# Performance work log

Hardware: AMD Instinct MI355X
Metric: run time of the kernel (lower is better)

Reference implementation:

```python
import jax, jax.numpy as jnp
import numpy as np

GROUP = 32  # values per quantization group (per-group scale)

def setup_inputs() -> dict:
    key = jax.random.key(0)
    k1, k2, k3, k4 = jax.random.split(key, 4)
    B, S, IN, OUT = 4, 2048, 4096, 4096
    x = jax.random.normal(k1, (B, S, IN), dtype=jnp.float32)
    # packed 4-bit weights: each int32 byte-value in [0,256) holds two nibbles
    w_packed = jax.random.randint(k2, (OUT, IN // 2), 0, 256, dtype=jnp.int32)
    scales = jax.random.uniform(k3, (OUT, IN // GROUP), dtype=jnp.float32) * 0.02 + 0.001
    bias = jax.random.normal(k4, (OUT,), dtype=jnp.float32)
    return {"x": x, "w_packed": w_packed, "scales": scales, "bias": bias}

def _dequantize(w_packed, scales):
    # w_packed: [OUT, IN//2] int32 bytes, scales: [OUT, IN//GROUP]
    OUT = w_packed.shape[0]
    low = w_packed & 0xF
    high = (w_packed >> 4) & 0xF
    q = jnp.stack([low, high], axis=-1).reshape(OUT, -1)  # [OUT, IN]
    qf = q.astype(jnp.float32) - 8.0  # signed 4-bit centered at 8
    qg = qf.reshape(OUT, scales.shape[1], GROUP)
    w = qg * scales[:, :, None]
    return w.reshape(OUT, -1)  # [OUT, IN]

def reference(x, w_packed, scales, bias):
    # dequantize weights then F.linear: y = x @ W^T + b
    W = _dequantize(w_packed, scales)  # [OUT, IN]
    y = jnp.einsum('bsi,oi->bso', x, W) + bias
    return y
```

## Files before the change

### kernel.cpp

```cpp
#include <hip/hip_runtime.h>
#include <stdint.h>

#define M_TOT 8192
#define K_TOT 4096
#define N_TOT 4096
#define GROUPQ 32

#define BM 256
#define BN 256
#define BK 32
#define NT (K_TOT / BK)

typedef __bf16 bf16x8 __attribute__((ext_vector_type(8)));
typedef float f32x4 __attribute__((ext_vector_type(4)));
typedef unsigned short u16;
typedef unsigned short u16x8 __attribute__((ext_vector_type(8)));

__device__ __forceinline__ u16 f2bf_rne(float f) {
  union { float f; uint32_t u; } v; v.f = f;
  uint32_t u = v.u;
  uint32_t r = (u + 0x7FFFu + ((u >> 16) & 1u)) >> 16;
  return (u16)r;
}

__global__ void cvt_x_kernel(const float* __restrict__ x, u16* __restrict__ xb, int n8) {
  int stride = gridDim.x * blockDim.x;
  for (int i = blockIdx.x * blockDim.x + threadIdx.x; i < n8; i += stride) {
    const float4* p = (const float4*)(x + (size_t)i * 8);
    float4 a = p[0];
    float4 b = p[1];
    u16x8 o;
    o[0] = f2bf_rne(a.x); o[1] = f2bf_rne(a.y); o[2] = f2bf_rne(a.z); o[3] = f2bf_rne(a.w);
    o[4] = f2bf_rne(b.x); o[5] = f2bf_rne(b.y); o[6] = f2bf_rne(b.z); o[7] = f2bf_rne(b.w);
    *(u16x8*)(xb + (size_t)i * 8) = o;
  }
}

__global__ void dequant_w_kernel(const int* __restrict__ wp, const float* __restrict__ sc,
                                 u16* __restrict__ wb) {
  const int KH = K_TOT / 2;
  const int total = N_TOT * KH / 8;
  int stride = gridDim.x * blockDim.x;
  for (int t = blockIdx.x * blockDim.x + threadIdx.x; t < total; t += stride) {
    int base = t * 8;
    int o = base >> 11;
    int ci = base & 2047;
    int e0 = ci * 2;
    float scale = sc[o * (K_TOT / GROUPQ) + (e0 >> 5)];
    int4 p0 = *(const int4*)(wp + base);
    int4 p1 = *(const int4*)(wp + base + 4);
    int v[8] = {p0.x, p0.y, p0.z, p0.w, p1.x, p1.y, p1.z, p1.w};
    u16x8 oA, oB;
#pragma unroll
    for (int j = 0; j < 8; ++j) {
      float lo = (float)((v[j] & 0xF) - 8) * scale;
      float hi = (float)(((v[j] >> 4) & 0xF) - 8) * scale;
      u16 lob = f2bf_rne(lo), hib = f2bf_rne(hi);
      if (j < 4) { oA[2 * j] = lob; oA[2 * j + 1] = hib; }
      else       { oB[2 * (j - 4)] = lob; oB[2 * (j - 4) + 1] = hib; }
    }
    u16* dst = wb + (size_t)o * K_TOT + e0;
    *(u16x8*)dst = oA;
    *(u16x8*)(dst + 8) = oB;
  }
}

__global__ __launch_bounds__(512, 2) void gemm_bf16_kernel(
    const u16* __restrict__ A, const u16* __restrict__ Bt,
    const float* __restrict__ bias, float* __restrict__ C) {
  __shared__ alignas(16) u16 sA[3][BM * BK];
  __shared__ alignas(16) u16 sB[3][BN * BK];

  const int ntn = N_TOT / BN;
  int wg = blockIdx.x, nwg = gridDim.x;
  int cpx = nwg >> 3;
  int swz = (wg & 7) * cpx + (wg >> 3);
  int bm = swz / ntn, bn = swz % ntn;

  int tid = threadIdx.x, wid = tid >> 6, lane = tid & 63;
  int wr = wid >> 2, wc = wid & 3;

  int srow0 = (wid * 2) * 16 + (lane >> 2);
  int srow1 = (wid * 2 + 1) * 16 + (lane >> 2);
  int cl = lane & 3;
  int gch0 = (cl ^ ((srow0 >> 1) & 3)) * 8;
  int gch1 = (cl ^ ((srow1 >> 1) & 3)) * 8;
  const u16* aS0 = A + (size_t)(bm * BM + srow0) * K_TOT + gch0;
  const u16* aS1 = A + (size_t)(bm * BM + srow1) * K_TOT + gch1;
  const u16* bS0 = Bt + (size_t)(bn * BN + srow0) * K_TOT + gch0;
  const u16* bS1 = Bt + (size_t)(bn * BN + srow1) * K_TOT + gch1;
  int ldst0 = (wid * 2) * 16 * BK;
  int ldst1 = (wid * 2 + 1) * 16 * BK;

  auto stageA = [&](int ke, int b) {
    __builtin_amdgcn_global_load_lds(
        (const __attribute__((address_space(1))) uint32_t*)(aS0 + ke),
        (__attribute__((address_space(3))) uint32_t*)(&sA[b][ldst0]), 16, 0, 0);
    __builtin_amdgcn_global_load_lds(
        (const __attribute__((address_space(1))) uint32_t*)(aS1 + ke),
        (__attribute__((address_space(3))) uint32_t*)(&sA[b][ldst1]), 16, 0, 0);
  };
  auto stageB = [&](int ke, int b) {
    __builtin_amdgcn_global_load_lds(
        (const __attribute__((address_space(1))) uint32_t*)(bS0 + ke),
        (__attribute__((address_space(3))) uint32_t*)(&sB[b][ldst0]), 16, 0, 0);
    __builtin_amdgcn_global_load_lds(
        (const __attribute__((address_space(1))) uint32_t*)(bS1 + ke),
        (__attribute__((address_space(3))) uint32_t*)(&sB[b][ldst1]), 16, 0, 0);
  };

  int rr = lane & 15, rc = lane >> 4;
  int xorv = (rc ^ ((rr >> 1) & 3)) * 8;
  int abase = (wr * 128 + rr) * BK + xorv;
  int bbase = (wc * 64 + rr) * BK + xorv;

  f32x4 acc[8][4] = {};

  stageA(0, 0); stageB(0, 0);
  stageA(BK, 1); stageB(BK, 1);
  asm volatile("s_waitcnt vmcnt(4)" ::: "memory");
  __builtin_amdgcn_s_barrier();

  for (int t = 0; t < NT; ++t) {
    int bt = t % 3;
    int bs = (t + 2) % 3;
    int ks = (t + 2) * BK;
    const u16* cA = sA[bt];
    const u16* cB = sB[bt];
    bool pf = (t + 2) < NT;

    bf16x8 bfr[4], af[4];
#pragma unroll
    for (int n = 0; n < 4; ++n) bfr[n] = *(const bf16x8*)(cB + bbase + n * 16 * BK);
#pragma unroll
    for (int m = 0; m < 4; ++m) af[m] = *(const bf16x8*)(cA + abase + m * 16 * BK);
    if (pf) stageA(ks, bs);
    __builtin_amdgcn_s_barrier();
    asm volatile("s_waitcnt lgkmcnt(0)" ::: "memory");
    __builtin_amdgcn_sched_barrier(0);
    __builtin_amdgcn_s_setprio(1);
#pragma unroll
    for (int m = 0; m < 4; ++m)
#pragma unroll
      for (int n = 0; n < 4; ++n)
        acc[m][n] = __builtin_amdgcn_mfma_f32_16x16x32_bf16(af[m], bfr[n], acc[m][n], 0, 0, 0);
    __builtin_amdgcn_s_setprio(0);
    __builtin_amdgcn_s_barrier();

#pragma unroll
    for (int m = 0; m < 4; ++m) af[m] = *(const bf16x8*)(cA + abase + (m + 4) * 16 * BK);
    if (pf) stageB(ks, bs);
    __builtin_amdgcn_s_barrier();
    asm volatile("s_waitcnt lgkmcnt(0)" ::: "memory");
    __builtin_amdgcn_sched_barrier(0);
    __builtin_amdgcn_s_setprio(1);
#pragma unroll
    for (int m = 0; m < 4; ++m)
#pragma unroll
      for (int n = 0; n < 4; ++n)
        acc[m + 4][n] = __builtin_amdgcn_mfma_f32_16x16x32_bf16(af[m], bfr[n], acc[m + 4][n], 0, 0, 0);
    __builtin_amdgcn_s_setprio(0);
    if (pf) { asm volatile("s_waitcnt vmcnt(4)" ::: "memory"); }
    else    { asm volatile("s_waitcnt vmcnt(0)" ::: "memory"); }
    __builtin_amdgcn_s_barrier();
  }

  int col = lane & 15;
  int rb = (lane >> 4) * 4;
#pragma unroll
  for (int n = 0; n < 4; ++n) {
    int gn = bn * BN + wc * 64 + n * 16 + col;
    float bsv = bias[gn];
#pragma unroll
    for (int m = 0; m < 8; ++m) {
      int gm = bm * BM + wr * 128 + m * 16 + rb;
#pragma unroll
      for (int j = 0; j < 4; ++j)
        C[(size_t)(gm + j) * N_TOT + gn] = acc[m][n][j] + bsv;
    }
  }
}

__global__ void fill_kernel(float* p, int n, float v) {
  int stride = gridDim.x * blockDim.x;
  for (int i = blockIdx.x * blockDim.x + threadIdx.x; i < n; i += stride) p[i] = v;
}

extern "C" void kernel_launch(void* const* d_in, const int* in_sizes, int n_in,
                              void* d_out, int out_size, void* d_ws, size_t ws_size,
                              hipStream_t stream) {
  const float* x = (const float*)d_in[0];
  const int* wp = (const int*)d_in[1];
  const float* sc = (const float*)d_in[2];
  const float* bias = (const float*)d_in[3];
  float* out = (float*)d_out;

  size_t xb_bytes = (size_t)M_TOT * K_TOT * 2;
  size_t wb_bytes = (size_t)N_TOT * K_TOT * 2;
  if (ws_size < xb_bytes + wb_bytes) {
    fill_kernel<<<2048, 256, 0, stream>>>(out, out_size, 12345.0f);
    return;
  }
  u16* xb = (u16*)d_ws;
  u16* wb = (u16*)((char*)d_ws + xb_bytes);

  cvt_x_kernel<<<2048, 256, 0, stream>>>(x, xb, M_TOT * K_TOT / 8);
  dequant_w_kernel<<<2048, 256, 0, stream>>>(wp, sc, wb);
  gemm_bf16_kernel<<<(M_TOT / BM) * (N_TOT / BN), 512, 0, stream>>>(xb, wb, bias, out);
}
```

Before: 313.3 us.

## Deepen GEMM LDS pipeline to four stages with register double-buffered fragments

```diff
diff --git a/kernel.cpp b/kernel.cpp
--- a/kernel.cpp
+++ b/kernel.cpp
@@ -68,8 +68,8 @@
 __global__ __launch_bounds__(512, 2) void gemm_bf16_kernel(
     const u16* __restrict__ A, const u16* __restrict__ Bt,
     const float* __restrict__ bias, float* __restrict__ C) {
-  __shared__ alignas(16) u16 sA[3][BM * BK];
-  __shared__ alignas(16) u16 sB[3][BN * BK];
+  __shared__ alignas(16) u16 sA[4][BM * BK];
+  __shared__ alignas(16) u16 sB[4][BN * BK];
 
   const int ntn = N_TOT / BN;
   int wg = blockIdx.x, nwg = gridDim.x;
@@ -118,51 +118,54 @@
 
   stageA(0, 0); stageB(0, 0);
   stageA(BK, 1); stageB(BK, 1);
-  asm volatile("s_waitcnt vmcnt(4)" ::: "memory");
+  stageA(2 * BK, 2); stageB(2 * BK, 2);
+  asm volatile("s_waitcnt vmcnt(8)" ::: "memory");
   __builtin_amdgcn_s_barrier();
 
+  bf16x8 afA[4], bfrA[4], afB[4], afN[4], bfrN[4];
+#pragma unroll
+  for (int n = 0; n < 4; ++n) bfrA[n] = *(const bf16x8*)(sB[0] + bbase + n * 16 * BK);
+#pragma unroll
+  for (int m = 0; m < 4; ++m) afA[m] = *(const bf16x8*)(sA[0] + abase + m * 16 * BK);
+
   for (int t = 0; t < NT; ++t) {
-    int bt = t % 3;
-    int bs = (t + 2) % 3;
-    int ks = (t + 2) * BK;
-    const u16* cA = sA[bt];
-    const u16* cB = sB[bt];
-    bool pf = (t + 2) < NT;
-
-    bf16x8 bfr[4], af[4];
-#pragma unroll
-    for (int n = 0; n < 4; ++n) bfr[n] = *(const bf16x8*)(cB + bbase + n * 16 * BK);
-#pragma unroll
-    for (int m = 0; m < 4; ++m) af[m] = *(const bf16x8*)(cA + abase + m * 16 * BK);
-    if (pf) stageA(ks, bs);
+    const u16* cA = sA[t & 3];
+    const u16* cB = sB[t & 3];
+    const u16* nA = sA[(t + 1) & 3];
+    const u16* nB = sB[(t + 1) & 3];
+    int bs = (t + 3) & 3;
+    int ks = ((t + 3 < NT) ? (t + 3) : (NT - 1)) * BK;
+    (void)cB;
+
     __builtin_amdgcn_s_barrier();
-    asm volatile("s_waitcnt lgkmcnt(0)" ::: "memory");
-    __builtin_amdgcn_sched_barrier(0);
+    stageA(ks, bs);
+#pragma unroll
+    for (int m = 0; m < 4; ++m) afB[m] = *(const bf16x8*)(cA + abase + (m + 4) * 16 * BK);
     __builtin_amdgcn_s_setprio(1);
 #pragma unroll
     for (int m = 0; m < 4; ++m)
 #pragma unroll
       for (int n = 0; n < 4; ++n)
-        acc[m][n] = __builtin_amdgcn_mfma_f32_16x16x32_bf16(af[m], bfr[n], acc[m][n], 0, 0, 0);
+        acc[m][n] = __builtin_amdgcn_mfma_f32_16x16x32_bf16(afA[m], bfrA[n], acc[m][n], 0, 0, 0);
     __builtin_amdgcn_s_setprio(0);
+
+    asm volatile("s_waitcnt vmcnt(6)" ::: "memory");
     __builtin_amdgcn_s_barrier();
-
-#pragma unroll
-    for (int m = 0; m < 4; ++m) af[m] = *(const bf16x8*)(cA + abase + (m + 4) * 16 * BK);
-    if (pf) stageB(ks, bs);
-    __builtin_amdgcn_s_barrier();
-    asm volatile("s_waitcnt lgkmcnt(0)" ::: "memory");
-    __builtin_amdgcn_sched_barrier(0);
+    stageB(ks, bs);
+#pragma unroll
+    for (int n = 0; n < 4; ++n) bfrN[n] = *(const bf16x8*)(nB + bbase + n * 16 * BK);
+#pragma unroll
+    for (int m = 0; m < 4; ++m) afN[m] = *(const bf16x8*)(nA + abase + m * 16 * BK);
     __builtin_amdgcn_s_setprio(1);
 #pragma unroll
     for (int m = 0; m < 4; ++m)
 #pragma unroll
       for (int n = 0; n < 4; ++n)
-        acc[m + 4][n] = __builtin_amdgcn_mfma_f32_16x16x32_bf16(af[m], bfr[n], acc[m + 4][n], 0, 0, 0);
+        acc[m + 4][n] = __builtin_amdgcn_mfma_f32_16x16x32_bf16(afB[m], bfrA[n], acc[m + 4][n], 0, 0, 0);
     __builtin_amdgcn_s_setprio(0);
-    if (pf) { asm volatile("s_waitcnt vmcnt(4)" ::: "memory"); }
-    else    { asm volatile("s_waitcnt vmcnt(0)" ::: "memory"); }
-    __builtin_amdgcn_s_barrier();
+
+#pragma unroll
+    for (int i = 0; i < 4; ++i) { afA[i] = afN[i]; bfrA[i] = bfrN[i]; }
   }
 
   int col = lane & 15;
```

Measured after the change: 397.0 us. +26.7%, slower.

## Switch GEMM to 32x32x16 MFMA tiles and single-phase K-loop

Applied to the files above, without the earlier changes.

```diff
diff --git a/kernel.cpp b/kernel.cpp
--- a/kernel.cpp
+++ b/kernel.cpp
@@ -12,7 +12,7 @@
 #define NT (K_TOT / BK)
 
 typedef __bf16 bf16x8 __attribute__((ext_vector_type(8)));
-typedef float f32x4 __attribute__((ext_vector_type(4)));
+typedef float f32x16 __attribute__((ext_vector_type(16)));
 typedef unsigned short u16;
 typedef unsigned short u16x8 __attribute__((ext_vector_type(8)));
 
@@ -109,12 +109,15 @@
         (__attribute__((address_space(3))) uint32_t*)(&sB[b][ldst1]), 16, 0, 0);
   };
 
-  int rr = lane & 15, rc = lane >> 4;
-  int xorv = (rc ^ ((rr >> 1) & 3)) * 8;
-  int abase = (wr * 128 + rr) * BK + xorv;
-  int bbase = (wc * 64 + rr) * BK + xorv;
-
-  f32x4 acc[8][4] = {};
+  int rl = lane & 31;
+  int kx = lane >> 5;
+  int rx = (lane >> 1) & 3;
+  int abase = (wr * 128 + rl) * BK;
+  int bbase = (wc * 64 + rl) * BK;
+  int ch0 = ((0 * 2 + kx) ^ rx) * 8;
+  int ch1 = ((1 * 2 + kx) ^ rx) * 8;
+
+  f32x16 acc[4][2] = {};
 
   stageA(0, 0); stageB(0, 0);
   stageA(BK, 1); stageB(BK, 1);
@@ -129,54 +132,51 @@
     const u16* cB = sB[bt];
     bool pf = (t + 2) < NT;
 
-    bf16x8 bfr[4], af[4];
-#pragma unroll
-    for (int n = 0; n < 4; ++n) bfr[n] = *(const bf16x8*)(cB + bbase + n * 16 * BK);
-#pragma unroll
-    for (int m = 0; m < 4; ++m) af[m] = *(const bf16x8*)(cA + abase + m * 16 * BK);
-    if (pf) stageA(ks, bs);
-    __builtin_amdgcn_s_barrier();
+    if (pf) { stageA(ks, bs); stageB(ks, bs); }
+
+    bf16x8 af[4][2], bfr[2][2];
+#pragma unroll
+    for (int m = 0; m < 4; ++m) {
+      af[m][0] = *(const bf16x8*)(cA + abase + m * 32 * BK + ch0);
+      af[m][1] = *(const bf16x8*)(cA + abase + m * 32 * BK + ch1);
+    }
+#pragma unroll
+    for (int n = 0; n < 2; ++n) {
+      bfr[n][0] = *(const bf16x8*)(cB + bbase + n * 32 * BK + ch0);
+      bfr[n][1] = *(const bf16x8*)(cB + bbase + n * 32 * BK + ch1);
+    }
+
     asm volatile("s_waitcnt lgkmcnt(0)" ::: "memory");
     __builtin_amdgcn_sched_barrier(0);
     __builtin_amdgcn_s_setprio(1);
 #pragma unroll
-    for (int m = 0; m < 4; ++m)
-#pragma unroll
-      for (int n = 0; n < 4; ++n)
-        acc[m][n] = __builtin_amdgcn_mfma_f32_16x16x32_bf16(af[m], bfr[n], acc[m][n], 0, 0, 0);
+    for (int kk = 0; kk < 2; ++kk)
+#pragma unroll
+      for (int m = 0; m < 4; ++m)
+#pragma unroll
+        for (int n = 0; n < 2; ++n)
+          acc[m][n] = __builtin_amdgcn_mfma_f32_32x32x16_bf16(af[m][kk], bfr[n][kk], acc[m][n], 0, 0, 0);
     __builtin_amdgcn_s_setprio(0);
-    __builtin_amdgcn_s_barrier();
-
-#pragma unroll
-    for (int m = 0; m < 4; ++m) af[m] = *(const bf16x8*)(cA + abase + (m + 4) * 16 * BK);
-    if (pf) stageB(ks, bs);
-    __builtin_amdgcn_s_barrier();
-    asm volatile("s_waitcnt lgkmcnt(0)" ::: "memory");
-    __builtin_amdgcn_sched_barrier(0);
-    __builtin_amdgcn_s_setprio(1);
-#pragma unroll
-    for (int m = 0; m < 4; ++m)
-#pragma unroll
-      for (int n = 0; n < 4; ++n)
-        acc[m + 4][n] = __builtin_amdgcn_mfma_f32_16x16x32_bf16(af[m], bfr[n], acc[m + 4][n], 0, 0, 0);
-    __builtin_amdgcn_s_setprio(0);
+
     if (pf) { asm volatile("s_waitcnt vmcnt(4)" ::: "memory"); }
     else    { asm volatile("s_waitcnt vmcnt(0)" ::: "memory"); }
     __builtin_amdgcn_s_barrier();
   }
 
-  int col = lane & 15;
-  int rb = (lane >> 4) * 4;
-#pragma unroll
-  for (int n = 0; n < 4; ++n) {
-    int gn = bn * BN + wc * 64 + n * 16 + col;
+  int colc = lane & 31;
+  int rquad = (lane >> 5) * 4;
+#pragma unroll
+  for (int n = 0; n < 2; ++n) {
+    int gn = bn * BN + wc * 64 + n * 32 + colc;
     float bsv = bias[gn];
 #pragma unroll
-    for (int m = 0; m < 8; ++m) {
-      int gm = bm * BM + wr * 128 + m * 16 + rb;
-#pragma unroll
-      for (int j = 0; j < 4; ++j)
-        C[(size_t)(gm + j) * N_TOT + gn] = acc[m][n][j] + bsv;
+    for (int m = 0; m < 4; ++m) {
+      int gmb = bm * BM + wr * 128 + m * 32;
+#pragma unroll
+      for (int reg = 0; reg < 16; ++reg) {
+        int row = (reg & 3) + 8 * (reg >> 2) + rquad;
+        C[(size_t)(gmb + row) * N_TOT + gn] = acc[m][n][reg] + bsv;
+      }
     }
   }
 }
```

After: 376.5 us. +20.2%, slower.

## Rework GEMM main loop into 4-phase double-buffered BK=64 pipeline with register prefetch

Applied to the files above, without the earlier changes.

```diff
diff --git a/kernel.cpp b/kernel.cpp
--- a/kernel.cpp
+++ b/kernel.cpp
@@ -8,7 +8,7 @@
 
 #define BM 256
 #define BN 256
-#define BK 32
+#define BK 64
 #define NT (K_TOT / BK)
 
 typedef __bf16 bf16x8 __attribute__((ext_vector_type(8)));
@@ -68,8 +68,7 @@
 __global__ __launch_bounds__(512, 2) void gemm_bf16_kernel(
     const u16* __restrict__ A, const u16* __restrict__ Bt,
     const float* __restrict__ bias, float* __restrict__ C) {
-  __shared__ alignas(16) u16 sA[3][BM * BK];
-  __shared__ alignas(16) u16 sB[3][BN * BK];
+  __shared__ alignas(16) u16 sL[65536];
 
   const int ntn = N_TOT / BN;
   int wg = blockIdx.x, nwg = gridDim.x;
@@ -79,91 +78,153 @@
 
   int tid = threadIdx.x, wid = tid >> 6, lane = tid & 63;
   int wr = wid >> 2, wc = wid & 3;
-
-  int srow0 = (wid * 2) * 16 + (lane >> 2);
-  int srow1 = (wid * 2 + 1) * 16 + (lane >> 2);
-  int cl = lane & 3;
-  int gch0 = (cl ^ ((srow0 >> 1) & 3)) * 8;
-  int gch1 = (cl ^ ((srow1 >> 1) & 3)) * 8;
-  const u16* aS0 = A + (size_t)(bm * BM + srow0) * K_TOT + gch0;
-  const u16* aS1 = A + (size_t)(bm * BM + srow1) * K_TOT + gch1;
-  const u16* bS0 = Bt + (size_t)(bn * BN + srow0) * K_TOT + gch0;
-  const u16* bS1 = Bt + (size_t)(bn * BN + srow1) * K_TOT + gch1;
-  int ldst0 = (wid * 2) * 16 * BK;
-  int ldst1 = (wid * 2 + 1) * 16 * BK;
-
-  auto stageA = [&](int ke, int b) {
-    __builtin_amdgcn_global_load_lds(
-        (const __attribute__((address_space(1))) uint32_t*)(aS0 + ke),
-        (__attribute__((address_space(3))) uint32_t*)(&sA[b][ldst0]), 16, 0, 0);
-    __builtin_amdgcn_global_load_lds(
-        (const __attribute__((address_space(1))) uint32_t*)(aS1 + ke),
-        (__attribute__((address_space(3))) uint32_t*)(&sA[b][ldst1]), 16, 0, 0);
-  };
-  auto stageB = [&](int ke, int b) {
-    __builtin_amdgcn_global_load_lds(
-        (const __attribute__((address_space(1))) uint32_t*)(bS0 + ke),
-        (__attribute__((address_space(3))) uint32_t*)(&sB[b][ldst0]), 16, 0, 0);
-    __builtin_amdgcn_global_load_lds(
-        (const __attribute__((address_space(1))) uint32_t*)(bS1 + ke),
-        (__attribute__((address_space(3))) uint32_t*)(&sB[b][ldst1]), 16, 0, 0);
-  };
-
-  int rr = lane & 15, rc = lane >> 4;
-  int xorv = (rc ^ ((rr >> 1) & 3)) * 8;
-  int abase = (wr * 128 + rr) * BK + xorv;
-  int bbase = (wc * 64 + rr) * BK + xorv;
+  const size_t K = K_TOT;
+
+  int rowS = tid >> 2;
+  int cgS = (tid & 3) ^ ((rowS >> 1) & 3);
+  const u16* pA = A + ((size_t)(bm * 256 + (rowS >> 6) * 128 + (rowS & 63))) * K + cgS * 8;
+  const u16* pB = Bt + ((size_t)(bn * 256 + (rowS >> 5) * 64 + (rowS & 31))) * K + cgS * 8;
+  u16* sE = &sL[0];
+
+  auto stA = [&](int T, int mh) {
+    int buf = T & 1;
+    const u16* s = pA + (size_t)mh * 64 * K + T * 64;
+    u16* d0 = sE + ((buf * 2 + 0) * 2 + mh) * 4096 + tid * 8;
+    u16* d1 = sE + ((buf * 2 + 1) * 2 + mh) * 4096 + tid * 8;
+    __builtin_amdgcn_global_load_lds(
+        (const __attribute__((address_space(1))) uint32_t*)s,
+        (__attribute__((address_space(3))) uint32_t*)d0, 16, 0, 0);
+    __builtin_amdgcn_global_load_lds(
+        (const __attribute__((address_space(1))) uint32_t*)(s + 32),
+        (__attribute__((address_space(3))) uint32_t*)d1, 16, 0, 0);
+  };
+  auto stB = [&](int T, int nh) {
+    int buf = T & 1;
+    const u16* s = pB + (size_t)nh * 32 * K + T * 64;
+    u16* d0 = sE + 32768 + ((buf * 2 + 0) * 2 + nh) * 4096 + tid * 8;
+    u16* d1 = sE + 32768 + ((buf * 2 + 1) * 2 + nh) * 4096 + tid * 8;
+    __builtin_amdgcn_global_load_lds(
+        (const __attribute__((address_space(1))) uint32_t*)s,
+        (__attribute__((address_space(3))) uint32_t*)d0, 16, 0, 0);
+    __builtin_amdgcn_global_load_lds(
+        (const __attribute__((address_space(1))) uint32_t*)(s + 32),
+        (__attribute__((address_space(3))) uint32_t*)d1, 16, 0, 0);
+  };
+
+  int rA = wr * 64 + (lane & 15);
+  int cA = ((lane >> 4) ^ ((rA >> 1) & 3)) * 8;
+  int rB = wc * 32 + (lane & 15);
+  int cB = ((lane >> 4) ^ ((rB >> 1) & 3)) * 8;
+  auto ldA = [&](int buf, int kk, int mh, int m3) {
+    return *(const bf16x8*)(sE + ((buf * 2 + kk) * 2 + mh) * 4096 + (rA + m3 * 16) * 32 + cA);
+  };
+  auto ldB = [&](int buf, int kk, int nh, int n2) {
+    return *(const bf16x8*)(sE + 32768 + ((buf * 2 + kk) * 2 + nh) * 4096 + (rB + n2 * 16) * 32 + cB);
+  };
 
   f32x4 acc[8][4] = {};
-
-  stageA(0, 0); stageB(0, 0);
-  stageA(BK, 1); stageB(BK, 1);
+  bf16x8 a0[4][2], a1[4][2], b0[2][2], b1[2][2];
+
+  stA(0, 0); stB(0, 0); stB(0, 1); stA(0, 1);
+  stA(1, 0); stB(1, 0); stB(1, 1); stA(1, 1);
   asm volatile("s_waitcnt vmcnt(4)" ::: "memory");
   __builtin_amdgcn_s_barrier();
 
+#pragma unroll
+  for (int m3 = 0; m3 < 4; ++m3)
+#pragma unroll
+    for (int kk = 0; kk < 2; ++kk) a0[m3][kk] = ldA(0, kk, 0, m3);
+#pragma unroll
+  for (int n2 = 0; n2 < 2; ++n2)
+#pragma unroll
+    for (int kk = 0; kk < 2; ++kk) b0[n2][kk] = ldB(0, kk, 0, n2);
+  asm volatile("s_waitcnt lgkmcnt(0)" ::: "memory");
+  __builtin_amdgcn_s_barrier();
+
   for (int t = 0; t < NT; ++t) {
-    int bt = t % 3;
-    int bs = (t + 2) % 3;
-    int ks = (t + 2) * BK;
-    const u16* cA = sA[bt];
-    const u16* cB = sB[bt];
-    bool pf = (t + 2) < NT;
-
-    bf16x8 bfr[4], af[4];
-#pragma unroll
-    for (int n = 0; n < 4; ++n) bfr[n] = *(const bf16x8*)(cB + bbase + n * 16 * BK);
-#pragma unroll
-    for (int m = 0; m < 4; ++m) af[m] = *(const bf16x8*)(cA + abase + m * 16 * BK);
-    if (pf) stageA(ks, bs);
-    __builtin_amdgcn_s_barrier();
+    int buf = t & 1;
+    int nbuf = buf ^ 1;
+    bool st_ok = (t + 2 < NT);
+    bool rd_ok = (t + 1 < NT);
+    int Ts = t + 2;
+
+#pragma unroll
+    for (int n2 = 0; n2 < 2; ++n2)
+#pragma unroll
+      for (int kk = 0; kk < 2; ++kk) b1[n2][kk] = ldB(buf, kk, 1, n2);
+    if (st_ok) stA(Ts, 0);
+    __builtin_amdgcn_s_barrier();
+    __builtin_amdgcn_s_setprio(1);
+#pragma unroll
+    for (int kk = 0; kk < 2; ++kk)
+#pragma unroll
+      for (int m3 = 0; m3 < 4; ++m3)
+#pragma unroll
+        for (int n2 = 0; n2 < 2; ++n2)
+          acc[m3][n2] = __builtin_amdgcn_mfma_f32_16x16x32_bf16(a0[m3][kk], b0[n2][kk], acc[m3][n2], 0, 0, 0);
+    __builtin_amdgcn_s_setprio(0);
+    __builtin_amdgcn_s_barrier();
+
+#pragma unroll
+    for (int m3 = 0; m3 < 4; ++m3)
+#pragma unroll
+      for (int kk = 0; kk < 2; ++kk) a1[m3][kk] = ldA(buf, kk, 1, m3);
+    if (st_ok) stB(Ts, 0);
+    __builtin_amdgcn_s_barrier();
+    __builtin_amdgcn_s_setprio(1);
+#pragma unroll
+    for (int kk = 0; kk < 2; ++kk)
+#pragma unroll
+      for (int m3 = 0; m3 < 4; ++m3)
+#pragma unroll
+        for (int n2 = 0; n2 < 2; ++n2)
+          acc[m3][n2 + 2] = __builtin_amdgcn_mfma_f32_16x16x32_bf16(a0[m3][kk], b1[n2][kk], acc[m3][n2 + 2], 0, 0, 0);
+    __builtin_amdgcn_s_setprio(0);
+    __builtin_amdgcn_s_barrier();
+
+    if (rd_ok) {
+#pragma unroll
+      for (int m3 = 0; m3 < 4; ++m3)
+#pragma unroll
+        for (int kk = 0; kk < 2; ++kk) a0[m3][kk] = ldA(nbuf, kk, 0, m3);
+    }
+    if (st_ok) stB(Ts, 1);
+    __builtin_amdgcn_s_barrier();
+    __builtin_amdgcn_s_setprio(1);
+#pragma unroll
+    for (int kk = 0; kk < 2; ++kk)
+#pragma unroll
+      for (int m3 = 0; m3 < 4; ++m3)
+#pragma unroll
+        for (int n2 = 0; n2 < 2; ++n2)
+          acc[m3 + 4][n2] = __builtin_amdgcn_mfma_f32_16x16x32_bf16(a1[m3][kk], b0[n2][kk], acc[m3 + 4][n2], 0, 0, 0);
+    __builtin_amdgcn_s_setprio(0);
+    __builtin_amdgcn_s_barrier();
+
+    if (rd_ok) {
+#pragma unroll
+      for (int n2 = 0; n2 < 2; ++n2)
+#pragma unroll
+        for (int kk = 0; kk < 2; ++kk) b0[n2][kk] = ldB(nbuf, kk, 0, n2);
+    }
+    if (st_ok) stA(Ts, 1);
+    __builtin_amdgcn_s_barrier();
+    __builtin_amdgcn_s_setprio(1);
+#pragma unroll
+    for (int kk = 0; kk < 2; ++kk)
+#pragma unroll
+      for (int m3 = 0; m3 < 4; ++m3)
+#pragma unroll
+        for (int n2 = 0; n2 < 2; ++n2)
+          acc[m3 + 4][n2 + 2] = __builtin_amdgcn_mfma_f32_16x16x32_bf16(a1[m3][kk], b1[n2][kk], acc[m3 + 4][n2 + 2], 0, 0, 0);
+    __builtin_amdgcn_s_setprio(0);
     asm volatile("s_waitcnt lgkmcnt(0)" ::: "memory");
-    __builtin_amdgcn_sched_barrier(0);
-    __builtin_amdgcn_s_setprio(1);
-#pragma unroll
-    for (int m = 0; m < 4; ++m)
-#pragma unroll
-      for (int n = 0; n < 4; ++n)
-        acc[m][n] = __builtin_amdgcn_mfma_f32_16x16x32_bf16(af[m], bfr[n], acc[m][n], 0, 0, 0);
-    __builtin_amdgcn_s_setprio(0);
-    __builtin_amdgcn_s_barrier();
-
-#pragma unroll
-    for (int m = 0; m < 4; ++m) af[m] = *(const bf16x8*)(cA + abase + (m + 4) * 16 * BK);
-    if (pf) stageB(ks, bs);
-    __builtin_amdgcn_s_barrier();
-    asm volatile("s_waitcnt lgkmcnt(0)" ::: "memory");
-    __builtin_amdgcn_sched_barrier(0);
-    __builtin_amdgcn_s_setprio(1);
-#pragma unroll
-    for (int m = 0; m < 4; ++m)
-#pragma unroll
-      for (int n = 0; n < 4; ++n)
-        acc[m + 4][n] = __builtin_amdgcn_mfma_f32_16x16x32_bf16(af[m], bfr[n], acc[m + 4][n], 0, 0, 0);
-    __builtin_amdgcn_s_setprio(0);
-    if (pf) { asm volatile("s_waitcnt vmcnt(4)" ::: "memory"); }
-    else    { asm volatile("s_waitcnt vmcnt(0)" ::: "memory"); }
-    __builtin_amdgcn_s_barrier();
-  }
+    if (t < NT - 2) { asm volatile("s_waitcnt vmcnt(4)" ::: "memory"); }
+    else            { asm volatile("s_waitcnt vmcnt(0)" ::: "memory"); }
+    __builtin_amdgcn_s_barrier();
+  }
+
+  asm volatile("s_waitcnt vmcnt(0)" ::: "memory");
 
   int col = lane & 15;
   int rb = (lane >> 4) * 4;
```

Result: faster. 279.4 us (-10.8%).
